# Kernel tuning notes

Measured on AMD Instinct MI355X. Metric: run time of the kernel, lower is better.

The kernel has to match this reference:

```python
import jax, jax.numpy as jnp
import numpy as np

D_MODEL = 1024
NUM_HEADS = 16
D_K = D_MODEL // NUM_HEADS
THETA = 10000.0
BATCH = 2
SEQ = 2048


def apply_rope(x, token_positions):
    # x: [B, H, S, D_K]; token_positions: [S] int
    half = D_K // 2
    inv_freq = THETA ** (-(jnp.arange(half, dtype=jnp.float32) * 2.0) / D_K)  # [half]
    angles = token_positions.astype(jnp.float32)[:, None] * inv_freq[None, :]  # [S, half]
    cos = jnp.cos(angles)  # [S, half]
    sin = jnp.sin(angles)
    x1 = x[..., 0::2]  # even indices
    x2 = x[..., 1::2]  # odd indices
    out_even = x1 * cos - x2 * sin
    out_odd = x1 * sin + x2 * cos
    # interleave back: [..., S, half, 2] -> [..., S, D_K]
    return jnp.stack([out_even, out_odd], axis=-1).reshape(x.shape)


def setup_inputs() -> dict:
    key = jax.random.key(0)
    ks = jax.random.split(key, 5)
    x = jax.random.normal(ks[0], (BATCH, SEQ, D_MODEL), dtype=jnp.float32)
    token_positions = jnp.arange(SEQ, dtype=jnp.int64)
    scale = 0.02
    Wq = jax.random.normal(ks[1], (D_MODEL, D_MODEL), dtype=jnp.float32) * scale
    Wk = jax.random.normal(ks[2], (D_MODEL, D_MODEL), dtype=jnp.float32) * scale
    Wv = jax.random.normal(ks[3], (D_MODEL, D_MODEL), dtype=jnp.float32) * scale
    Wo = jax.random.normal(ks[4], (D_MODEL, D_MODEL), dtype=jnp.float32) * scale
    return {"x": x, "token_positions": token_positions, "Wq": Wq, "Wk": Wk, "Wv": Wv, "Wo": Wo}


def reference(x, token_positions, Wq, Wk, Wv, Wo):
    B, S, _ = x.shape
    # cs336 Linear: y = x @ W.T with W of shape (out, in), no bias
    def proj(W):
        h = jnp.einsum('bsd,od->bso', x, W)
        return h.reshape(B, S, NUM_HEADS, D_K).transpose(0, 2, 1, 3)  # [B,H,S,Dk]
    Q = apply_rope(proj(Wq), token_positions)
    K = apply_rope(proj(Wk), token_positions)
    V = proj(Wv)
    scores = jnp.einsum('bhqd,bhkd->bhqk', Q, K) / jnp.sqrt(jnp.float32(D_K))
    causal = jnp.tril(jnp.ones((S, S), dtype=bool))
    scores = jnp.where(causal, scores, -jnp.inf)
    attn = jax.nn.softmax(scores, axis=-1)
    out = jnp.einsum('bhqk,bhkd->bhqd', attn, V)  # [B,H,S,Dk]
    out = out.transpose(0, 2, 1, 3).reshape(B, S, D_MODEL)
    return jnp.einsum('bsd,od->bso', out, Wo)
```

## Files before the change

### kernel.cpp

```cpp
#include <hip/hip_runtime.h>
#include <hip/hip_bf16.h>
#include <math.h>

#define NHEADS 16
#define DKH 64
#define SEQ 2048
#define DMODEL 1024

typedef __attribute__((ext_vector_type(8))) short short8;
typedef __attribute__((ext_vector_type(4))) float f32x4;

#define GLDS16(g, l)                                         \
  __builtin_amdgcn_global_load_lds(                          \
      (__attribute__((address_space(1))) void*)(void*)(g),   \
      (__attribute__((address_space(3))) void*)(l), 16, 0, 0)

__device__ __forceinline__ short f2bf(float f) {
  unsigned u = __float_as_uint(f);
  unsigned r = (u + 0x7fffu + ((u >> 16) & 1u)) >> 16;
  return (short)r;
}

__device__ __forceinline__ unsigned cvtpk(float lo, float hi) {
  unsigned r;
  asm("v_cvt_pk_bf16_f32 %0, %1, %2" : "=v"(r) : "v"(lo), "v"(hi));
  return r;
}

__device__ __forceinline__ short8 pack8(float4 a, float4 b) {
  short8 v;
  v[0] = f2bf(a.x); v[1] = f2bf(a.y); v[2] = f2bf(a.z); v[3] = f2bf(a.w);
  v[4] = f2bf(b.x); v[5] = f2bf(b.y); v[6] = f2bf(b.z); v[7] = f2bf(b.w);
  return v;
}

__device__ __forceinline__ int swz(int r, int gran) {
  return r * 64 + ((gran ^ (r & 7)) << 3);
}

__global__ __launch_bounds__(256) void precast_rope_kernel(
    const float* __restrict__ X, const float* __restrict__ Wq,
    const float* __restrict__ Wk, const float* __restrict__ Wv,
    const float* __restrict__ Wo, const int* __restrict__ tp,
    short* __restrict__ Xb, short* __restrict__ Wqb, short* __restrict__ Wkb,
    short* __restrict__ Wvb, short* __restrict__ Wob,
    float* __restrict__ ct, float* __restrict__ st) {
  int bid = blockIdx.x;
  if (bid < 4096) {
    int i = bid * 256 + threadIdx.x;
    const float* src; short* dst; int off;
    if (i < 524288) { src = X; dst = Xb; off = i; }
    else {
      int k = i - 524288; int w = k >> 17; off = k & 131071;
      src = (w == 0) ? Wq : (w == 1) ? Wk : (w == 2) ? Wv : Wo;
      dst = (w == 0) ? Wqb : (w == 1) ? Wkb : (w == 2) ? Wvb : Wob;
    }
    const float4* p = reinterpret_cast<const float4*>(src) + 2 * (size_t)off;
    float4 a = p[0], b = p[1];
    reinterpret_cast<short8*>(dst)[off] = pack8(a, b);
  } else {
    int idx = (bid - 4096) * 256 + threadIdx.x;
    if (idx >= SEQ * 32) return;
    int s = idx >> 5, i = idx & 31;
    int is64 = (tp[1] == 0);
    int p = is64 ? tp[2 * s] : tp[s];
    float invf = powf(10000.0f, -(2.0f * (float)i) / 64.0f);
    float a = (float)p * invf;
    ct[idx] = cosf(a);
    st[idx] = sinf(a);
  }
}

__global__ __launch_bounds__(256) void gemm_qkv_kernel(
    const short* __restrict__ X, const short* __restrict__ Wq,
    const short* __restrict__ Wk, const short* __restrict__ Wv,
    short* __restrict__ Qb, short* __restrict__ Kb, short* __restrict__ Vb,
    const float* __restrict__ ct, const float* __restrict__ st) {
  __shared__ __align__(16) short As[128 * 64];
  __shared__ __align__(16) short Bs[128 * 64];
  const int tm = blockIdx.x;
  const int tn = blockIdx.y;
  const int tid = threadIdx.x;
  const int wave = tid >> 6, lane = tid & 63;
  const int l15 = lane & 15, quad = lane >> 4;
  const int wm = wave >> 1, wn = wave & 1;

  const int mid = tn >> 3;
  const int n0 = (tn & 7) * 128;
  const short* W = (mid == 0) ? Wq : (mid == 1 ? Wk : Wv);
  const short* Abase = X + (size_t)(tm * 128) * DMODEL;
  const short* Bbase = W + (size_t)n0 * DMODEL;

  const int lr = lane >> 3;
  const int lc = (lane & 7) ^ lr;

  f32x4 acc[4][4];
#pragma unroll
  for (int mb = 0; mb < 4; mb++)
#pragma unroll
    for (int nb = 0; nb < 4; nb++) acc[mb][nb] = (f32x4){0.f, 0.f, 0.f, 0.f};

  for (int kk = 0; kk < 16; kk++) {
    const short* Ak = Abase + kk * 64;
    const short* Bk = Bbase + kk * 64;
#pragma unroll
    for (int i = 0; i < 4; i++) {
      int R = i * 32 + wave * 8;
      GLDS16(Ak + (size_t)(R + lr) * DMODEL + lc * 8, &As[R * 64 + lane * 8]);
    }
#pragma unroll
    for (int i = 0; i < 4; i++) {
      int R = i * 32 + wave * 8;
      GLDS16(Bk + (size_t)(R + lr) * DMODEL + lc * 8, &Bs[R * 64 + lane * 8]);
    }
    __syncthreads();
#pragma unroll
    for (int kg = 0; kg < 2; kg++) {
      short8 af[4], bf[4];
#pragma unroll
      for (int mb = 0; mb < 4; mb++) {
        int r = wm * 64 + mb * 16 + l15;
        af[mb] = *reinterpret_cast<const short8*>(&As[swz(r, kg * 4 + quad)]);
      }
#pragma unroll
      for (int nb = 0; nb < 4; nb++) {
        int r = wn * 64 + nb * 16 + l15;
        bf[nb] = *reinterpret_cast<const short8*>(&Bs[swz(r, kg * 4 + quad)]);
      }
#pragma unroll
      for (int mb = 0; mb < 4; mb++)
#pragma unroll
        for (int nb = 0; nb < 4; nb++)
          acc[mb][nb] = __builtin_amdgcn_mfma_f32_16x16x32_bf16(af[mb], bf[nb], acc[mb][nb], 0, 0, 0);
    }
    __syncthreads();
  }

#pragma unroll
  for (int mb = 0; mb < 4; mb++) {
    const int s0g = tm * 128 + wm * 64 + mb * 16 + quad * 4;
    const int b = s0g >> 11, s = s0g & 2047;
#pragma unroll
    for (int nb = 0; nb < 4; nb++) {
      int nl = n0 + wn * 64 + nb * 16 + l15;
      int h = nl >> 6, dd = nl & 63;
      if (mid == 2) {
        unsigned u0 = (unsigned)(unsigned short)f2bf(acc[mb][nb][0]) |
                      ((unsigned)(unsigned short)f2bf(acc[mb][nb][1]) << 16);
        unsigned u1 = (unsigned)(unsigned short)f2bf(acc[mb][nb][2]) |
                      ((unsigned)(unsigned short)f2bf(acc[mb][nb][3]) << 16);
        uint2 pk; pk.x = u0; pk.y = u1;
        *reinterpret_cast<uint2*>(Vb + ((size_t)(b * NHEADS + h) * DKH + dd) * SEQ + s) = pk;
      } else {
#pragma unroll
        for (int reg = 0; reg < 4; reg++) {
          float v = acc[mb][nb][reg];
          float pv = __shfl_xor(v, 1);
          int fi = dd >> 1;
          int sg = s + reg;
          float c = ct[sg * 32 + fi], sn = st[sg * 32 + fi];
          float o = (dd & 1) ? (pv * sn + v * c) : (v * c - pv * sn);
          size_t oi = (((size_t)(b * NHEADS + h)) * SEQ + sg) * DKH + dd;
          ((mid == 0) ? Qb : Kb)[oi] = f2bf(o);
        }
      }
    }
  }
}

__global__ __launch_bounds__(256, 4) void attn_kernel(
    const short* __restrict__ Qb, const short* __restrict__ Kb,
    const short* __restrict__ Vtb, short* __restrict__ Ob) {
  __shared__ __align__(16) short Ks[2][64 * 64];
  __shared__ __align__(16) short Vs[2][64 * 64];

  const int id = blockIdx.x;
  const int x8 = id & 7;
  const int c  = (id >> 3) & 31;
  const int q2 = id >> 8;
  const int bh = x8 * 4 + q2;
  const int qt = (q2 == 0) ? c
               : (q2 == 1) ? (31 - c)
               : (q2 == 2) ? ((c + 16) & 31)
               : ((15 - c) & 31);

  const int tid = threadIdx.x;
  const int wave = tid >> 6, lane = tid & 63;
  const int l15 = lane & 15, quad = lane >> 4;
  const int sr0 = tid >> 3, sc = tid & 7;

  const int vga = ((sc >> 2) << 2) + ((sc & 1) << 1);
  const int vh4 = ((sc >> 1) & 1) * 4;

  const short* Qp = Qb + (size_t)bh * SEQ * DKH;
  const short* Kp = Kb + (size_t)bh * SEQ * DKH;
  const short* Vp = Vtb + (size_t)bh * DKH * SEQ;

  uint4 kreg[2], vreg[2];
#pragma unroll
  for (int i = 0; i < 2; i++) {
    int r = sr0 + i * 32;
    kreg[i] = *reinterpret_cast<const uint4*>(Kp + (size_t)r * DKH + sc * 8);
    vreg[i] = *reinterpret_cast<const uint4*>(Vp + (size_t)r * SEQ + sc * 8);
  }
  short8 qf0, qf1;
  {
    const short* qrow = Qp + (size_t)(qt * 64 + wave * 16 + l15) * DKH;
    qf0 = *reinterpret_cast<const short8*>(qrow + quad * 8);
    qf1 = *reinterpret_cast<const short8*>(qrow + (4 + quad) * 8);
  }
#pragma unroll
  for (int i = 0; i < 2; i++) {
    int r = sr0 + i * 32;
    *reinterpret_cast<uint4*>(&Ks[0][swz(r, sc)]) = kreg[i];
    uint2 lo, hi;
    lo.x = vreg[i].x; lo.y = vreg[i].y; hi.x = vreg[i].z; hi.y = vreg[i].w;
    *reinterpret_cast<uint2*>(&Vs[0][swz(r, vga) + vh4]) = lo;
    *reinterpret_cast<uint2*>(&Vs[0][swz(r, vga + 1) + vh4]) = hi;
  }
  __syncthreads();

  f32x4 accO[4];
#pragma unroll
  for (int i = 0; i < 4; i++) accO[i] = (f32x4){0.f, 0.f, 0.f, 0.f};
  float rs = 0.f;

  const float SCL = 0.125f * 1.44269504089f;
  const float FM = 13.0f;

  int buf = 0;
  for (int kt = 0; kt <= qt; kt++) {
    if (kt < qt) {
#pragma unroll
      for (int i = 0; i < 2; i++) {
        int r = sr0 + i * 32;
        kreg[i] = *reinterpret_cast<const uint4*>(Kp + (size_t)((kt + 1) * 64 + r) * DKH + sc * 8);
        vreg[i] = *reinterpret_cast<const uint4*>(Vp + (size_t)r * SEQ + (kt + 1) * 64 + sc * 8);
      }
    }

    f32x4 sa[4];
    __builtin_amdgcn_s_setprio(1);
#pragma unroll
    for (int nb = 0; nb < 4; nb++) {
      sa[nb] = (f32x4){0.f, 0.f, 0.f, 0.f};
      int r = nb * 16 + l15;
      short8 kf0 = *reinterpret_cast<const short8*>(&Ks[buf][swz(r, quad)]);
      sa[nb] = __builtin_amdgcn_mfma_f32_16x16x32_bf16(kf0, qf0, sa[nb], 0, 0, 0);
      short8 kf1 = *reinterpret_cast<const short8*>(&Ks[buf][swz(r, 4 + quad)]);
      sa[nb] = __builtin_amdgcn_mfma_f32_16x16x32_bf16(kf1, qf1, sa[nb], 0, 0, 0);
    }
    __builtin_amdgcn_s_setprio(0);

    const bool diag = (kt == qt);
    const int prow = wave * 16 + l15;
    unsigned pu[4], pw[4];
#pragma unroll
    for (int nb = 0; nb < 4; nb++) {
      float p0 = exp2f(sa[nb][0] * SCL - FM);
      float p1 = exp2f(sa[nb][1] * SCL - FM);
      float p2 = exp2f(sa[nb][2] * SCL - FM);
      float p3 = exp2f(sa[nb][3] * SCL - FM);
      if (diag) {
        int kbase = nb * 16 + quad * 4;
        if (kbase + 0 > prow) p0 = 0.f;
        if (kbase + 1 > prow) p1 = 0.f;
        if (kbase + 2 > prow) p2 = 0.f;
        if (kbase + 3 > prow) p3 = 0.f;
      }
      rs += (p0 + p1) + (p2 + p3);
      pu[nb] = cvtpk(p0, p1);
      pw[nb] = cvtpk(p2, p3);
    }

    short8 pf0, pf1;
    {
      unsigned* w0 = reinterpret_cast<unsigned*>(&pf0);
      w0[0] = pu[0]; w0[1] = pw[0]; w0[2] = pu[1]; w0[3] = pw[1];
      unsigned* w1 = reinterpret_cast<unsigned*>(&pf1);
      w1[0] = pu[2]; w1[1] = pw[2]; w1[2] = pu[3]; w1[3] = pw[3];
    }
    __builtin_amdgcn_s_setprio(1);
#pragma unroll
    for (int db = 0; db < 4; db++) {
      int dv = db * 16 + l15;
      short8 vf0 = *reinterpret_cast<const short8*>(&Vs[buf][swz(dv, quad)]);
      accO[db] = __builtin_amdgcn_mfma_f32_16x16x32_bf16(pf0, vf0, accO[db], 0, 0, 0);
      short8 vf1 = *reinterpret_cast<const short8*>(&Vs[buf][swz(dv, 4 + quad)]);
      accO[db] = __builtin_amdgcn_mfma_f32_16x16x32_bf16(pf1, vf1, accO[db], 0, 0, 0);
    }
    __builtin_amdgcn_s_setprio(0);

    if (kt < qt) {
      int nbuf = buf ^ 1;
#pragma unroll
      for (int i = 0; i < 2; i++) {
        int r = sr0 + i * 32;
        *reinterpret_cast<uint4*>(&Ks[nbuf][swz(r, sc)]) = kreg[i];
        uint2 lo, hi;
        lo.x = vreg[i].x; lo.y = vreg[i].y; hi.x = vreg[i].z; hi.y = vreg[i].w;
        *reinterpret_cast<uint2*>(&Vs[nbuf][swz(r, vga) + vh4]) = lo;
        *reinterpret_cast<uint2*>(&Vs[nbuf][swz(r, vga + 1) + vh4]) = hi;
      }
      __syncthreads();
      buf = nbuf;
    }
  }

  float t = rs;
  t += __shfl_xor(t, 16);
  t += __shfl_xor(t, 32);
  float lv[4];
#pragma unroll
  for (int reg = 0; reg < 4; reg++) lv[reg] = __shfl(t, quad * 4 + reg);

  int b = bh >> 4, h = bh & 15;
#pragma unroll
  for (int db = 0; db < 4; db++)
#pragma unroll
    for (int reg = 0; reg < 4; reg++) {
      int s = qt * 64 + wave * 16 + quad * 4 + reg;
      int dv = db * 16 + l15;
      float o = accO[db][reg] / lv[reg];
      Ob[((size_t)(b * SEQ + s)) * DMODEL + h * DKH + dv] = f2bf(o);
    }
}

__global__ __launch_bounds__(256) void gemm_out_kernel(
    const short* __restrict__ X, const short* __restrict__ Wo, float* __restrict__ Out) {
  __shared__ __align__(16) short As[2][128 * 64];
  __shared__ __align__(16) short Bs[2][64 * 64];
  const int tm = blockIdx.x;
  const int tn = blockIdx.y;
  const int tid = threadIdx.x;
  const int wave = tid >> 6, lane = tid & 63;
  const int l15 = lane & 15, quad = lane >> 4;
  const int wm = wave >> 1, wn = wave & 1;

  const short* Abase = X + (size_t)(tm * 128) * DMODEL;
  const short* Bbase = Wo + (size_t)(tn * 64) * DMODEL;

  const int lr = lane >> 3;
  const int lc = (lane & 7) ^ lr;

  f32x4 acc[4][2];
#pragma unroll
  for (int mb = 0; mb < 4; mb++)
#pragma unroll
    for (int nb = 0; nb < 2; nb++) acc[mb][nb] = (f32x4){0.f, 0.f, 0.f, 0.f};

  for (int ko = 0; ko < 8; ko++) {
    const short* Ak = Abase + ko * 128;
    const short* Bk = Bbase + ko * 128;
#pragma unroll
    for (int h = 0; h < 2; h++) {
#pragma unroll
      for (int i = 0; i < 4; i++) {
        int R = i * 32 + wave * 8;
        GLDS16(Ak + (size_t)(R + lr) * DMODEL + h * 64 + lc * 8,
               &As[h][R * 64 + lane * 8]);
      }
#pragma unroll
      for (int i = 0; i < 2; i++) {
        int R = i * 32 + wave * 8;
        GLDS16(Bk + (size_t)(R + lr) * DMODEL + h * 64 + lc * 8,
               &Bs[h][R * 64 + lane * 8]);
      }
    }
    __syncthreads();
#pragma unroll
    for (int h = 0; h < 2; h++) {
#pragma unroll
      for (int kg = 0; kg < 2; kg++) {
        short8 af[4], bf[2];
#pragma unroll
        for (int mb = 0; mb < 4; mb++) {
          int r = wm * 64 + mb * 16 + l15;
          af[mb] = *reinterpret_cast<const short8*>(&As[h][swz(r, kg * 4 + quad)]);
        }
#pragma unroll
        for (int nb = 0; nb < 2; nb++) {
          int r = wn * 32 + nb * 16 + l15;
          bf[nb] = *reinterpret_cast<const short8*>(&Bs[h][swz(r, kg * 4 + quad)]);
        }
#pragma unroll
        for (int mb = 0; mb < 4; mb++)
#pragma unroll
          for (int nb = 0; nb < 2; nb++)
            acc[mb][nb] = __builtin_amdgcn_mfma_f32_16x16x32_bf16(af[mb], bf[nb], acc[mb][nb], 0, 0, 0);
      }
    }
    __syncthreads();
  }
#pragma unroll
  for (int mb = 0; mb < 4; mb++)
#pragma unroll
    for (int nb = 0; nb < 2; nb++)
#pragma unroll
      for (int reg = 0; reg < 4; reg++) {
        int rg = tm * 128 + wm * 64 + mb * 16 + quad * 4 + reg;
        int col = tn * 64 + wn * 32 + nb * 16 + l15;
        Out[(size_t)rg * DMODEL + col] = acc[mb][nb][reg];
      }
}

extern "C" void kernel_launch(void* const* d_in, const int* in_sizes, int n_in,
                              void* d_out, int out_size, void* d_ws, size_t ws_size,
                              hipStream_t stream) {
  (void)in_sizes; (void)n_in; (void)out_size; (void)ws_size;
  const float* X  = (const float*)d_in[0];
  const int*   tp = (const int*)d_in[1];
  const float* Wq = (const float*)d_in[2];
  const float* Wk = (const float*)d_in[3];
  const float* Wv = (const float*)d_in[4];
  const float* Wo = (const float*)d_in[5];
  float* Out = (float*)d_out;

  short* Qb  = (short*)d_ws;
  short* Kb  = Qb + 4194304;
  short* Vb  = Kb + 4194304;
  short* Ab  = Vb + 4194304;
  short* Xb  = Ab + 4194304;
  short* Wqb = Xb + 4194304;
  short* Wkb = Wqb + 1048576;
  short* Wvb = Wkb + 1048576;
  short* Wob = Wvb + 1048576;
  float* ct  = (float*)(Wob + 1048576);
  float* st  = ct + SEQ * 32;

  precast_rope_kernel<<<dim3(4352), dim3(256), 0, stream>>>(
      X, Wq, Wk, Wv, Wo, tp, Xb, Wqb, Wkb, Wvb, Wob, ct, st);
  gemm_qkv_kernel<<<dim3(32, 24), dim3(256), 0, stream>>>(Xb, Wqb, Wkb, Wvb,
                                                          Qb, Kb, Vb, ct, st);
  attn_kernel<<<dim3(1024), dim3(256), 0, stream>>>(Qb, Kb, Vb, Ab);
  gemm_out_kernel<<<dim3(32, 16), dim3(256), 0, stream>>>(Ab, Wob, Out);
}
```

Measured before the change: 186.3 us.

## Load K/V tile pairs via direct-to-LDS copies and shrink out-proj GEMM K-step

The attention kernel drops its register-staged double buffer, where the next K/V tile was prefetched during compute. It now loads two consecutive 64-key tiles at once, K through global_load_lds straight into shared memory and V through registers, then computes both tiles between two barriers. This cuts barrier count and register pressure, but global loads no longer overlap the MFMA work. The output-projection GEMM goes from a 128-wide K step with two LDS halves to a 64-wide step with a single buffer, halving its LDS footprint in exchange for twice as many barrier-separated iterations.

```diff
diff --git a/kernel.cpp b/kernel.cpp
--- a/kernel.cpp
+++ b/kernel.cpp
@@ -188,6 +188,8 @@
   const int wave = tid >> 6, lane = tid & 63;
   const int l15 = lane & 15, quad = lane >> 4;
   const int sr0 = tid >> 3, sc = tid & 7;
+  const int lr = lane >> 3;
+  const int lc = (lane & 7) ^ lr;
 
   const int vga = ((sc >> 2) << 2) + ((sc & 1) << 1);
   const int vh4 = ((sc >> 1) & 1) * 4;
@@ -196,29 +198,12 @@
   const short* Kp = Kb + (size_t)bh * SEQ * DKH;
   const short* Vp = Vtb + (size_t)bh * DKH * SEQ;
 
-  uint4 kreg[2], vreg[2];
-#pragma unroll
-  for (int i = 0; i < 2; i++) {
-    int r = sr0 + i * 32;
-    kreg[i] = *reinterpret_cast<const uint4*>(Kp + (size_t)r * DKH + sc * 8);
-    vreg[i] = *reinterpret_cast<const uint4*>(Vp + (size_t)r * SEQ + sc * 8);
-  }
   short8 qf0, qf1;
   {
     const short* qrow = Qp + (size_t)(qt * 64 + wave * 16 + l15) * DKH;
     qf0 = *reinterpret_cast<const short8*>(qrow + quad * 8);
     qf1 = *reinterpret_cast<const short8*>(qrow + (4 + quad) * 8);
   }
-#pragma unroll
-  for (int i = 0; i < 2; i++) {
-    int r = sr0 + i * 32;
-    *reinterpret_cast<uint4*>(&Ks[0][swz(r, sc)]) = kreg[i];
-    uint2 lo, hi;
-    lo.x = vreg[i].x; lo.y = vreg[i].y; hi.x = vreg[i].z; hi.y = vreg[i].w;
-    *reinterpret_cast<uint2*>(&Vs[0][swz(r, vga) + vh4]) = lo;
-    *reinterpret_cast<uint2*>(&Vs[0][swz(r, vga + 1) + vh4]) = hi;
-  }
-  __syncthreads();
 
   f32x4 accO[4];
 #pragma unroll
@@ -227,84 +212,98 @@
 
   const float SCL = 0.125f * 1.44269504089f;
   const float FM = 13.0f;
-
-  int buf = 0;
-  for (int kt = 0; kt <= qt; kt++) {
-    if (kt < qt) {
-#pragma unroll
-      for (int i = 0; i < 2; i++) {
-        int r = sr0 + i * 32;
-        kreg[i] = *reinterpret_cast<const uint4*>(Kp + (size_t)((kt + 1) * 64 + r) * DKH + sc * 8);
-        vreg[i] = *reinterpret_cast<const uint4*>(Vp + (size_t)r * SEQ + (kt + 1) * 64 + sc * 8);
-      }
-    }
-
-    f32x4 sa[4];
-    __builtin_amdgcn_s_setprio(1);
-#pragma unroll
-    for (int nb = 0; nb < 4; nb++) {
-      sa[nb] = (f32x4){0.f, 0.f, 0.f, 0.f};
-      int r = nb * 16 + l15;
-      short8 kf0 = *reinterpret_cast<const short8*>(&Ks[buf][swz(r, quad)]);
-      sa[nb] = __builtin_amdgcn_mfma_f32_16x16x32_bf16(kf0, qf0, sa[nb], 0, 0, 0);
-      short8 kf1 = *reinterpret_cast<const short8*>(&Ks[buf][swz(r, 4 + quad)]);
-      sa[nb] = __builtin_amdgcn_mfma_f32_16x16x32_bf16(kf1, qf1, sa[nb], 0, 0, 0);
-    }
-    __builtin_amdgcn_s_setprio(0);
-
-    const bool diag = (kt == qt);
-    const int prow = wave * 16 + l15;
-    unsigned pu[4], pw[4];
-#pragma unroll
-    for (int nb = 0; nb < 4; nb++) {
-      float p0 = exp2f(sa[nb][0] * SCL - FM);
-      float p1 = exp2f(sa[nb][1] * SCL - FM);
-      float p2 = exp2f(sa[nb][2] * SCL - FM);
-      float p3 = exp2f(sa[nb][3] * SCL - FM);
-      if (diag) {
-        int kbase = nb * 16 + quad * 4;
-        if (kbase + 0 > prow) p0 = 0.f;
-        if (kbase + 1 > prow) p1 = 0.f;
-        if (kbase + 2 > prow) p2 = 0.f;
-        if (kbase + 3 > prow) p3 = 0.f;
-      }
-      rs += (p0 + p1) + (p2 + p3);
-      pu[nb] = cvtpk(p0, p1);
-      pw[nb] = cvtpk(p2, p3);
-    }
-
-    short8 pf0, pf1;
+  const int prow = wave * 16 + l15;
+  const int npairs = (qt + 2) >> 1;
+
+  for (int p = 0; p < npairs; p++) {
+    const int base = p * 128;
+#pragma unroll
+    for (int i = 0; i < 4; i++) {
+      int R = i * 32 + wave * 8;
+      GLDS16(Kp + (size_t)(base + R + lr) * DKH + lc * 8,
+             &Ks[R >> 6][(R & 63) * 64 + lane * 8]);
+    }
     {
-      unsigned* w0 = reinterpret_cast<unsigned*>(&pf0);
-      w0[0] = pu[0]; w0[1] = pw[0]; w0[2] = pu[1]; w0[3] = pw[1];
-      unsigned* w1 = reinterpret_cast<unsigned*>(&pf1);
-      w1[0] = pu[2]; w1[1] = pw[2]; w1[2] = pu[3]; w1[3] = pw[3];
-    }
-    __builtin_amdgcn_s_setprio(1);
-#pragma unroll
-    for (int db = 0; db < 4; db++) {
-      int dv = db * 16 + l15;
-      short8 vf0 = *reinterpret_cast<const short8*>(&Vs[buf][swz(dv, quad)]);
-      accO[db] = __builtin_amdgcn_mfma_f32_16x16x32_bf16(pf0, vf0, accO[db], 0, 0, 0);
-      short8 vf1 = *reinterpret_cast<const short8*>(&Vs[buf][swz(dv, 4 + quad)]);
-      accO[db] = __builtin_amdgcn_mfma_f32_16x16x32_bf16(pf1, vf1, accO[db], 0, 0, 0);
-    }
-    __builtin_amdgcn_s_setprio(0);
-
-    if (kt < qt) {
-      int nbuf = buf ^ 1;
-#pragma unroll
-      for (int i = 0; i < 2; i++) {
-        int r = sr0 + i * 32;
-        *reinterpret_cast<uint4*>(&Ks[nbuf][swz(r, sc)]) = kreg[i];
-        uint2 lo, hi;
-        lo.x = vreg[i].x; lo.y = vreg[i].y; hi.x = vreg[i].z; hi.y = vreg[i].w;
-        *reinterpret_cast<uint2*>(&Vs[nbuf][swz(r, vga) + vh4]) = lo;
-        *reinterpret_cast<uint2*>(&Vs[nbuf][swz(r, vga + 1) + vh4]) = hi;
-      }
-      __syncthreads();
-      buf = nbuf;
-    }
+      uint4 vr[2][2];
+#pragma unroll
+      for (int i = 0; i < 2; i++)
+#pragma unroll
+        for (int hs = 0; hs < 2; hs++) {
+          int r = sr0 + i * 32;
+          vr[i][hs] = *reinterpret_cast<const uint4*>(
+              Vp + (size_t)r * SEQ + base + hs * 64 + sc * 8);
+        }
+#pragma unroll
+      for (int i = 0; i < 2; i++)
+#pragma unroll
+        for (int hs = 0; hs < 2; hs++) {
+          int r = sr0 + i * 32;
+          uint2 lo, hi;
+          lo.x = vr[i][hs].x; lo.y = vr[i][hs].y;
+          hi.x = vr[i][hs].z; hi.y = vr[i][hs].w;
+          *reinterpret_cast<uint2*>(&Vs[hs][swz(r, vga) + vh4]) = lo;
+          *reinterpret_cast<uint2*>(&Vs[hs][swz(r, vga + 1) + vh4]) = hi;
+        }
+    }
+    __syncthreads();
+
+#pragma unroll
+    for (int s = 0; s < 2; s++) {
+      const int t = 2 * p + s;
+      if (t <= qt) {
+        f32x4 sa[4];
+        __builtin_amdgcn_s_setprio(1);
+#pragma unroll
+        for (int nb = 0; nb < 4; nb++) {
+          sa[nb] = (f32x4){0.f, 0.f, 0.f, 0.f};
+          int r = nb * 16 + l15;
+          short8 kf0 = *reinterpret_cast<const short8*>(&Ks[s][swz(r, quad)]);
+          sa[nb] = __builtin_amdgcn_mfma_f32_16x16x32_bf16(kf0, qf0, sa[nb], 0, 0, 0);
+          short8 kf1 = *reinterpret_cast<const short8*>(&Ks[s][swz(r, 4 + quad)]);
+          sa[nb] = __builtin_amdgcn_mfma_f32_16x16x32_bf16(kf1, qf1, sa[nb], 0, 0, 0);
+        }
+        __builtin_amdgcn_s_setprio(0);
+
+        const bool diag = (t == qt);
+        unsigned pu[4], pw[4];
+#pragma unroll
+        for (int nb = 0; nb < 4; nb++) {
+          float p0 = exp2f(sa[nb][0] * SCL - FM);
+          float p1 = exp2f(sa[nb][1] * SCL - FM);
+          float p2 = exp2f(sa[nb][2] * SCL - FM);
+          float p3 = exp2f(sa[nb][3] * SCL - FM);
+          if (diag) {
+            int kbase = nb * 16 + quad * 4;
+            if (kbase + 0 > prow) p0 = 0.f;
+            if (kbase + 1 > prow) p1 = 0.f;
+            if (kbase + 2 > prow) p2 = 0.f;
+            if (kbase + 3 > prow) p3 = 0.f;
+          }
+          rs += (p0 + p1) + (p2 + p3);
+          pu[nb] = cvtpk(p0, p1);
+          pw[nb] = cvtpk(p2, p3);
+        }
+
+        short8 pf0, pf1;
+        {
+          unsigned* w0 = reinterpret_cast<unsigned*>(&pf0);
+          w0[0] = pu[0]; w0[1] = pw[0]; w0[2] = pu[1]; w0[3] = pw[1];
+          unsigned* w1 = reinterpret_cast<unsigned*>(&pf1);
+          w1[0] = pu[2]; w1[1] = pw[2]; w1[2] = pu[3]; w1[3] = pw[3];
+        }
+        __builtin_amdgcn_s_setprio(1);
+#pragma unroll
+        for (int db = 0; db < 4; db++) {
+          int dv = db * 16 + l15;
+          short8 vf0 = *reinterpret_cast<const short8*>(&Vs[s][swz(dv, quad)]);
+          accO[db] = __builtin_amdgcn_mfma_f32_16x16x32_bf16(pf0, vf0, accO[db], 0, 0, 0);
+          short8 vf1 = *reinterpret_cast<const short8*>(&Vs[s][swz(dv, 4 + quad)]);
+          accO[db] = __builtin_amdgcn_mfma_f32_16x16x32_bf16(pf1, vf1, accO[db], 0, 0, 0);
+        }
+        __builtin_amdgcn_s_setprio(0);
+      }
+    }
+    __syncthreads();
   }
 
   float t = rs;
@@ -328,8 +327,8 @@
 
 __global__ __launch_bounds__(256) void gemm_out_kernel(
     const short* __restrict__ X, const short* __restrict__ Wo, float* __restrict__ Out) {
-  __shared__ __align__(16) short As[2][128 * 64];
-  __shared__ __align__(16) short Bs[2][64 * 64];
+  __shared__ __align__(16) short As[128 * 64];
+  __shared__ __align__(16) short Bs[64 * 64];
   const int tm = blockIdx.x;
   const int tn = blockIdx.y;
   const int tid = threadIdx.x;
@@ -349,46 +348,38 @@
 #pragma unroll
     for (int nb = 0; nb < 2; nb++) acc[mb][nb] = (f32x4){0.f, 0.f, 0.f, 0.f};
 
-  for (int ko = 0; ko < 8; ko++) {
-    const short* Ak = Abase + ko * 128;
-    const short* Bk = Bbase + ko * 128;
-#pragma unroll
-    for (int h = 0; h < 2; h++) {
-#pragma unroll
-      for (int i = 0; i < 4; i++) {
-        int R = i * 32 + wave * 8;
-        GLDS16(Ak + (size_t)(R + lr) * DMODEL + h * 64 + lc * 8,
-               &As[h][R * 64 + lane * 8]);
-      }
-#pragma unroll
-      for (int i = 0; i < 2; i++) {
-        int R = i * 32 + wave * 8;
-        GLDS16(Bk + (size_t)(R + lr) * DMODEL + h * 64 + lc * 8,
-               &Bs[h][R * 64 + lane * 8]);
-      }
-    }
-    __syncthreads();
-#pragma unroll
-    for (int h = 0; h < 2; h++) {
-#pragma unroll
-      for (int kg = 0; kg < 2; kg++) {
-        short8 af[4], bf[2];
-#pragma unroll
-        for (int mb = 0; mb < 4; mb++) {
-          int r = wm * 64 + mb * 16 + l15;
-          af[mb] = *reinterpret_cast<const short8*>(&As[h][swz(r, kg * 4 + quad)]);
-        }
-#pragma unroll
-        for (int nb = 0; nb < 2; nb++) {
-          int r = wn * 32 + nb * 16 + l15;
-          bf[nb] = *reinterpret_cast<const short8*>(&Bs[h][swz(r, kg * 4 + quad)]);
-        }
-#pragma unroll
-        for (int mb = 0; mb < 4; mb++)
-#pragma unroll
-          for (int nb = 0; nb < 2; nb++)
-            acc[mb][nb] = __builtin_amdgcn_mfma_f32_16x16x32_bf16(af[mb], bf[nb], acc[mb][nb], 0, 0, 0);
-      }
+  for (int kk = 0; kk < 16; kk++) {
+    const short* Ak = Abase + kk * 64;
+    const short* Bk = Bbase + kk * 64;
+#pragma unroll
+    for (int i = 0; i < 4; i++) {
+      int R = i * 32 + wave * 8;
+      GLDS16(Ak + (size_t)(R + lr) * DMODEL + lc * 8, &As[R * 64 + lane * 8]);
+    }
+#pragma unroll
+    for (int i = 0; i < 2; i++) {
+      int R = i * 32 + wave * 8;
+      GLDS16(Bk + (size_t)(R + lr) * DMODEL + lc * 8, &Bs[R * 64 + lane * 8]);
+    }
+    __syncthreads();
+#pragma unroll
+    for (int kg = 0; kg < 2; kg++) {
+      short8 af[4], bf[2];
+#pragma unroll
+      for (int mb = 0; mb < 4; mb++) {
+        int r = wm * 64 + mb * 16 + l15;
+        af[mb] = *reinterpret_cast<const short8*>(&As[swz(r, kg * 4 + quad)]);
+      }
+#pragma unroll
+      for (int nb = 0; nb < 2; nb++) {
+        int r = wn * 32 + nb * 16 + l15;
+        bf[nb] = *reinterpret_cast<const short8*>(&Bs[swz(r, kg * 4 + quad)]);
+      }
+#pragma unroll
+      for (int mb = 0; mb < 4; mb++)
+#pragma unroll
+        for (int nb = 0; nb < 2; nb++)
+          acc[mb][nb] = __builtin_amdgcn_mfma_f32_16x16x32_bf16(af[mb], bf[nb], acc[mb][nb], 0, 0, 0);
     }
     __syncthreads();
   }
```

After: 184.7 us. No clear change (-0.8%).
